# Performance work log

Measured on AMD Instinct MI355X. Metric: run time of the kernel, lower is better.

The kernel has to match this reference:

```python
import jax, jax.numpy as jnp
import numpy as np

B, N, M = 16, 4096, 1024
INPUT_DIM, COND_DIM = 512, 512
HEADS, DIM_HEAD = 8, 64
HIDDEN = HEADS * DIM_HEAD


def setup_inputs() -> dict:
    key = jax.random.key(0)
    ks = jax.random.split(key, 6)
    x = jax.random.normal(ks[0], (B, INPUT_DIM, N), dtype=jnp.float32)
    c = jax.random.normal(ks[1], (B, COND_DIM, M), dtype=jnp.float32)
    # 1x1 conv weights as [out_ch, in_ch] matrices
    Wq = jax.random.normal(ks[2], (HIDDEN, INPUT_DIM), dtype=jnp.float32) * (INPUT_DIM ** -0.5)
    Wkv = jax.random.normal(ks[3], (2 * HIDDEN, COND_DIM), dtype=jnp.float32) * (COND_DIM ** -0.5)
    Wo = jax.random.normal(ks[4], (INPUT_DIM, HIDDEN), dtype=jnp.float32) * (HIDDEN ** -0.5)
    bo = jax.random.normal(ks[5], (INPUT_DIM,), dtype=jnp.float32) * 0.01
    return {"x": x, "c": c, "Wq": Wq, "Wkv": Wkv, "Wo": Wo, "bo": bo}


def reference(x, c, Wq, Wkv, Wo, bo):
    scale = DIM_HEAD ** -0.5
    # 1x1 convs == channel-mixing matmuls
    q = jnp.einsum('bcn,oc->bon', x, Wq)            # [B, HIDDEN, N]
    kv = jnp.einsum('bcm,oc->bom', c, Wkv)          # [B, 2*HIDDEN, M]
    k, v = jnp.split(kv, 2, axis=1)                 # each [B, HIDDEN, M]
    # split heads: b (h d) n -> b h d n
    q = q.reshape(B, HEADS, DIM_HEAD, N) * scale
    k = k.reshape(B, HEADS, DIM_HEAD, M)
    v = v.reshape(B, HEADS, DIM_HEAD, M)
    # softmax over conditioning sequence dim
    k = jax.nn.softmax(k, axis=-1)
    # context: [B, H, d, e] (dim_head x dim_head)
    context = jnp.einsum('bhdm,bhem->bhde', k, v)
    # out: [B, H, e, N]
    out = jnp.einsum('bhde,bhdn->bhen', context, q)
    out = out.reshape(B, HIDDEN, N)
    return jnp.einsum('bcn,oc->bon', out, Wo) + bo[None, :, None]
```

## Files before the change

### kernel.cpp

```cpp
#include <hip/hip_runtime.h>

#define KDIM 512

typedef __attribute__((ext_vector_type(8))) short bf16x8;
typedef __attribute__((ext_vector_type(4))) float f32x4;
typedef unsigned short u16;
typedef unsigned int u32;

static __device__ __forceinline__ u16 f2bf(float f) {
  u32 u = __builtin_bit_cast(u32, f);
  u32 r = u + 0x7fffu + ((u >> 16) & 1u);
  return (u16)(r >> 16);
}
static __device__ __forceinline__ bf16x8 ld_frag(const u16* p) {
  uint2 lo = *(const uint2*)p;
  uint2 hi = *(const uint2*)(p + 4);
  uint4 u = make_uint4(lo.x, lo.y, hi.x, hi.y);
  return __builtin_bit_cast(bf16x8, u);
}

__global__ __launch_bounds__(256) void cvt_f32_bf16(
    const float* __restrict__ src, u16* __restrict__ dst, int n8)
{
  int i = blockIdx.x * 256 + threadIdx.x;
  if (i >= n8) return;
  float4 a = *(const float4*)(src + (long)i * 8);
  float4 b = *(const float4*)(src + (long)i * 8 + 4);
  u32 w0 = (u32)f2bf(a.x) | ((u32)f2bf(a.y) << 16);
  u32 w1 = (u32)f2bf(a.z) | ((u32)f2bf(a.w) << 16);
  u32 w2 = (u32)f2bf(b.x) | ((u32)f2bf(b.y) << 16);
  u32 w3 = (u32)f2bf(b.z) | ((u32)f2bf(b.w) << 16);
  *(uint4*)(dst + (long)i * 8) = make_uint4(w0, w1, w2, w3);
}

template<bool OUT_BF16, bool BIAS, bool CLUST>
__global__ __launch_bounds__(512, 2) void gemm_bm512(
    const u16* __restrict__ Ap, long a_bstride,
    const float* __restrict__ Bp, long b_bstride,
    void* __restrict__ Op, long o_bstride,
    const float* __restrict__ bias, int ldn)
{
  constexpr int LDT = 68;
  __shared__ u16 Ash[512 * LDT];
  __shared__ u16 Bsh[128 * LDT];

  int mt, nt, b;
  if constexpr (CLUST) {
    const int bx = blockIdx.x;
    const int xcd = bx & 7, idx = bx >> 3;
    b = xcd + 8 * (idx >> 5);
    nt = idx & 31;
    mt = 0;
  } else {
    mt = blockIdx.x; nt = blockIdx.y; b = blockIdx.z;
  }
  const long mtile = (long)mt * 512;
  const long ntile = (long)nt * 128;
  const u16* Ab = Ap + (long)b * a_bstride + mtile * KDIM;
  const float* Bb = Bp + (long)b * b_bstride + ntile;

  const int t = threadIdx.x;
  const int lane = t & 63, wv = t >> 6;
  const int wm = wv >> 1, wn = wv & 1;
  const int lrow = lane & 15, lkh = lane >> 4;

  const int arow = t >> 3, akc = t & 7;
  const int nq = t & 31;
  const int kq = ((t >> 5) ^ ((t >> 2) & 7)) & 15;

  f32x4 acc[8][4] = {};
  uint4 pa[8];
  float4 pb[4];

  #pragma unroll
  for (int i = 0; i < 8; ++i)
    pa[i] = *(const uint4*)(Ab + (long)(arow + i * 64) * KDIM + akc * 8);
  #pragma unroll
  for (int kk = 0; kk < 4; ++kk)
    pb[kk] = *(const float4*)(Bb + (long)(kq * 4 + kk) * ldn + nq * 4);

  #pragma unroll
  for (int i = 0; i < 8; ++i) {
    u16* dst = &Ash[(arow + i * 64) * LDT + akc * 8];
    *(uint2*)dst       = make_uint2(pa[i].x, pa[i].y);
    *(uint2*)(dst + 4) = make_uint2(pa[i].z, pa[i].w);
  }
  {
    float r0[4] = {pb[0].x, pb[0].y, pb[0].z, pb[0].w};
    float r1[4] = {pb[1].x, pb[1].y, pb[1].z, pb[1].w};
    float r2[4] = {pb[2].x, pb[2].y, pb[2].z, pb[2].w};
    float r3[4] = {pb[3].x, pb[3].y, pb[3].z, pb[3].w};
    #pragma unroll
    for (int jj = 0; jj < 4; ++jj) {
      u32 w0 = (u32)f2bf(r0[jj]) | ((u32)f2bf(r1[jj]) << 16);
      u32 w1 = (u32)f2bf(r2[jj]) | ((u32)f2bf(r3[jj]) << 16);
      *(uint2*)&Bsh[(nq * 4 + jj) * LDT + kq * 4] = make_uint2(w0, w1);
    }
  }
  __syncthreads();

  for (int kt8 = 0; kt8 < 8; ++kt8) {
    const bool more = kt8 < 7;
    if (more) {
      const int kt = (kt8 + 1) * 64;
      #pragma unroll
      for (int i = 0; i < 8; ++i)
        pa[i] = *(const uint4*)(Ab + (long)(arow + i * 64) * KDIM + kt + akc * 8);
      #pragma unroll
      for (int kk = 0; kk < 4; ++kk)
        pb[kk] = *(const float4*)(Bb + (long)(kt + kq * 4 + kk) * ldn + nq * 4);
    }
    #pragma unroll
    for (int kk = 0; kk < 2; ++kk) {
      bf16x8 bfr[4];
      #pragma unroll
      for (int ni = 0; ni < 4; ++ni)
        bfr[ni] = ld_frag(&Bsh[(wn * 64 + ni * 16 + lrow) * LDT + kk * 32 + lkh * 8]);
      #pragma unroll
      for (int mi = 0; mi < 8; ++mi) {
        bf16x8 af = ld_frag(&Ash[(wm * 128 + mi * 16 + lrow) * LDT + kk * 32 + lkh * 8]);
        #pragma unroll
        for (int ni = 0; ni < 4; ++ni)
          acc[mi][ni] = __builtin_amdgcn_mfma_f32_16x16x32_bf16(af, bfr[ni], acc[mi][ni], 0, 0, 0);
      }
    }
    __syncthreads();
    if (more) {
      #pragma unroll
      for (int i = 0; i < 8; ++i) {
        u16* dst = &Ash[(arow + i * 64) * LDT + akc * 8];
        *(uint2*)dst       = make_uint2(pa[i].x, pa[i].y);
        *(uint2*)(dst + 4) = make_uint2(pa[i].z, pa[i].w);
      }
      float r0[4] = {pb[0].x, pb[0].y, pb[0].z, pb[0].w};
      float r1[4] = {pb[1].x, pb[1].y, pb[1].z, pb[1].w};
      float r2[4] = {pb[2].x, pb[2].y, pb[2].z, pb[2].w};
      float r3[4] = {pb[3].x, pb[3].y, pb[3].z, pb[3].w};
      #pragma unroll
      for (int jj = 0; jj < 4; ++jj) {
        u32 w0 = (u32)f2bf(r0[jj]) | ((u32)f2bf(r1[jj]) << 16);
        u32 w1 = (u32)f2bf(r2[jj]) | ((u32)f2bf(r3[jj]) << 16);
        *(uint2*)&Bsh[(nq * 4 + jj) * LDT + kq * 4] = make_uint2(w0, w1);
      }
      __syncthreads();
    }
  }

  #pragma unroll
  for (int mi = 0; mi < 8; ++mi) {
    #pragma unroll
    for (int r = 0; r < 4; ++r) {
      long gr = mtile + wm * 128 + mi * 16 + lkh * 4 + r;
      float bv = 0.0f;
      if constexpr (BIAS) bv = bias[gr];
      #pragma unroll
      for (int ni = 0; ni < 4; ++ni) {
        long gc = ntile + wn * 64 + ni * 16 + lrow;
        float v = acc[mi][ni][r] + bv;
        if constexpr (OUT_BF16)
          ((u16*)Op)[(long)b * o_bstride + gr * ldn + gc] = f2bf(v);
        else
          ((float*)Op)[(long)b * o_bstride + gr * ldn + gc] = v;
      }
    }
  }
}

__global__ __launch_bounds__(256, 2) void softmax_context(
    const u16* __restrict__ kv, float* __restrict__ ctx)
{
  constexpr int LDE = 132;
  __shared__ float rowmax[64], rowinv[64];
  __shared__ u16 Ke[64 * LDE];
  __shared__ u16 Vs[64 * LDE];
  __shared__ float pr[64 * 68];

  const int bh = blockIdx.x;
  const u16* Kr = kv + (long)(bh >> 3) * (1024 * 1024) + (long)(bh & 7) * (64 * 1024);
  const u16* Vr = Kr + 512 * 1024;

  const int t = threadIdx.x;
  const int lane = t & 63, wv = t >> 6;
  const int lrow = lane & 15, lkh = lane >> 4;
  const int d4 = t >> 2, q4 = t & 3;

  {
    const u16* row = Kr + d4 * 1024 + q4 * 256;
    float mx = -3e38f;
    for (int i = 0; i < 256; i += 8) {
      uint4 v = *(const uint4*)(row + i);
      u32 ws[4] = {v.x, v.y, v.z, v.w};
      #pragma unroll
      for (int j = 0; j < 4; ++j) {
        mx = fmaxf(mx, __builtin_bit_cast(float, ws[j] << 16));
        mx = fmaxf(mx, __builtin_bit_cast(float, ws[j] & 0xffff0000u));
      }
    }
    mx = fmaxf(mx, __shfl_xor(mx, 1));
    mx = fmaxf(mx, __shfl_xor(mx, 2));
    float s = 0.f;
    for (int i = 0; i < 256; i += 8) {
      uint4 v = *(const uint4*)(row + i);
      u32 ws[4] = {v.x, v.y, v.z, v.w};
      #pragma unroll
      for (int j = 0; j < 4; ++j) {
        s += __expf(__builtin_bit_cast(float, ws[j] << 16) - mx);
        s += __expf(__builtin_bit_cast(float, ws[j] & 0xffff0000u) - mx);
      }
    }
    s += __shfl_xor(s, 1);
    s += __shfl_xor(s, 2);
    if (q4 == 0) { rowmax[d4] = mx; rowinv[d4] = 1.f / s; }
  }
  __syncthreads();

  f32x4 cacc[4][4] = {};

  for (int mc = 0; mc < 8; ++mc) {
    {
      int dd = t >> 2, j = t & 3;
      int m0 = mc * 128 + j * 32;
      float mx = rowmax[dd], inv = rowinv[dd];
      const u16* src = Kr + dd * 1024 + m0;
      u16* dst = &Ke[dd * LDE + j * 32];
      #pragma unroll
      for (int cq = 0; cq < 4; ++cq) {
        uint4 v = *(const uint4*)(src + cq * 8);
        u32 in[4] = {v.x, v.y, v.z, v.w};
        u32 out[4];
        #pragma unroll
        for (int j2 = 0; j2 < 4; ++j2) {
          float lo = __builtin_bit_cast(float, in[j2] << 16);
          float hi = __builtin_bit_cast(float, in[j2] & 0xffff0000u);
          out[j2] = (u32)f2bf(__expf(lo - mx) * inv) |
                    ((u32)f2bf(__expf(hi - mx) * inv) << 16);
        }
        *(uint2*)(dst + cq * 8)     = make_uint2(out[0], out[1]);
        *(uint2*)(dst + cq * 8 + 4) = make_uint2(out[2], out[3]);
      }
      const u16* vsrc = Vr + dd * 1024 + m0;
      u16* vdst = &Vs[dd * LDE + j * 32];
      #pragma unroll
      for (int cq = 0; cq < 4; ++cq) {
        uint4 v = *(const uint4*)(vsrc + cq * 8);
        *(uint2*)(vdst + cq * 8)     = make_uint2(v.x, v.y);
        *(uint2*)(vdst + cq * 8 + 4) = make_uint2(v.z, v.w);
      }
    }
    __syncthreads();
    bf16x8 ka[4], vb[4];
    #pragma unroll
    for (int mi = 0; mi < 4; ++mi)
      ka[mi] = ld_frag(&Ke[(mi * 16 + lrow) * LDE + wv * 32 + lkh * 8]);
    #pragma unroll
    for (int ni = 0; ni < 4; ++ni)
      vb[ni] = ld_frag(&Vs[(ni * 16 + lrow) * LDE + wv * 32 + lkh * 8]);
    #pragma unroll
    for (int mi = 0; mi < 4; ++mi)
      #pragma unroll
      for (int ni = 0; ni < 4; ++ni)
        cacc[mi][ni] = __builtin_amdgcn_mfma_f32_16x16x32_bf16(ka[mi], vb[ni], cacc[mi][ni], 0, 0, 0);
    __syncthreads();
  }

  for (int w = 0; w < 4; ++w) {
    if (wv == w) {
      #pragma unroll
      for (int mi = 0; mi < 4; ++mi)
        #pragma unroll
        for (int ni = 0; ni < 4; ++ni)
          #pragma unroll
          for (int r = 0; r < 4; ++r) {
            float* p = &pr[(mi * 16 + lkh * 4 + r) * 68 + (ni * 16 + lrow)];
            float v = cacc[mi][ni][r];
            if (w == 0) *p = v; else *p += v;
          }
    }
    __syncthreads();
  }
  float* cg = ctx + (long)bh * 4096;
  for (int i = 0; i < 16; ++i) {
    int o = t + i * 256;
    cg[o] = 0.125f * pr[(o >> 6) * 68 + (o & 63)];
  }
}

__global__ __launch_bounds__(256) void compose_u(
    const float* __restrict__ ctx, const float* __restrict__ Wo, u16* __restrict__ U)
{
  __shared__ float cs[16 * 64];
  const int bh = blockIdx.x, dq = blockIdx.y;
  const int b = bh >> 3, h = bh & 7;
  const int t = threadIdx.x;
  const float* cgrp = ctx + (long)bh * 4096 + dq * 16 * 64;
  for (int i = t; i < 1024; i += 256) cs[i] = cgrp[i];
  __syncthreads();
  #pragma unroll
  for (int rep = 0; rep < 2; ++rep) {
    int o = rep * 256 + t;
    const float* wrow = Wo + (long)o * 512 + h * 64;
    float acc[16] = {};
    for (int e = 0; e < 64; ++e) {
      float w = wrow[e];
      #pragma unroll
      for (int dd = 0; dd < 16; ++dd) acc[dd] += w * cs[dd * 64 + e];
    }
    u16* urow = U + (long)b * (512 * 512) + (long)o * 512 + h * 64 + dq * 16;
    #pragma unroll
    for (int dd = 0; dd < 16; ++dd) urow[dd] = f2bf(acc[dd]);
  }
}

extern "C" void kernel_launch(void* const* d_in, const int* in_sizes, int n_in,
                              void* d_out, int out_size, void* d_ws, size_t ws_size,
                              hipStream_t stream)
{
  const float* x   = (const float*)d_in[0];
  const float* c   = (const float*)d_in[1];
  const float* Wq  = (const float*)d_in[2];
  const float* Wkv = (const float*)d_in[3];
  const float* Wo  = (const float*)d_in[4];
  const float* bo  = (const float*)d_in[5];

  char* ws = (char*)d_ws;
  u16*   kv   = (u16*)ws;
  float* ctx  = (float*)(ws + 33554432);
  u16*   U    = (u16*)(ws + 35651584);
  u16*   Weff = (u16*)(ws + 44040192);
  u16*   Wkvb = (u16*)(ws + 44040192);

  cvt_f32_bf16<<<dim3(256), 256, 0, stream>>>(Wkv, Wkvb, 65536);
  gemm_bm512<true, false, false><<<dim3(2, 8, 16), 512, 0, stream>>>(
      Wkvb, 0, c, 512L * 1024, kv, 1024L * 1024, nullptr, 1024);
  softmax_context<<<dim3(128), 256, 0, stream>>>(kv, ctx);
  compose_u<<<dim3(128, 4), 256, 0, stream>>>(ctx, Wo, U);
  gemm_bm512<true, false, false><<<dim3(1, 4, 16), 512, 0, stream>>>(
      U, 512L * 512, Wq, 0, Weff, 512L * 512, nullptr, 512);
  gemm_bm512<false, true, true><<<dim3(512), 512, 0, stream>>>(
      Weff, 512L * 512, x, 512L * 4096, d_out, 512L * 4096, bo, 4096);
}
```

Before: 189.2 us.

## Rewrite GEMM with double-buffered swizzled LDS, wave priority, and staged epilogue

Replaces the single-buffer padded LDS GEMM with a 32-wide-K double-buffered pipeline. Tiles are stored with an XOR swizzle so fragments load as single 128-bit LDS reads. MFMA blocks are wrapped in s_setprio. The epilogue now stages accumulators through LDS so global stores are row-contiguous and vectorized, which targets the scattered scalar output writes. In exchange it uses more LDS (80KB) and adds extra barriers in the epilogue.

```diff
diff --git a/kernel.cpp b/kernel.cpp
--- a/kernel.cpp
+++ b/kernel.cpp
@@ -11,12 +11,6 @@
   u32 u = __builtin_bit_cast(u32, f);
   u32 r = u + 0x7fffu + ((u >> 16) & 1u);
   return (u16)(r >> 16);
-}
-static __device__ __forceinline__ bf16x8 ld_frag(const u16* p) {
-  uint2 lo = *(const uint2*)p;
-  uint2 hi = *(const uint2*)(p + 4);
-  uint4 u = make_uint4(lo.x, lo.y, hi.x, hi.y);
-  return __builtin_bit_cast(bf16x8, u);
 }
 
 __global__ __launch_bounds__(256) void cvt_f32_bf16(
@@ -33,27 +27,60 @@
   *(uint4*)(dst + (long)i * 8) = make_uint4(w0, w1, w2, w3);
 }
 
+#define AOFF(row, c16) ((((row) * 32) + (c16)) ^ (((row) & 7) << 3))
+
+#define LOADA(dst, kt) { _Pragma("unroll") \
+  for (int i_ = 0; i_ < 4; ++i_) \
+    dst[i_] = *(const uint4*)(Ab + (long)(ar + i_ * 128) * KDIM + (kt) + ac * 8); }
+
+#define LOADB(d0, d1, kt) { \
+  d0 = *(const float4*)(Bb + (long)((kt) + kq2)     * ldn + nq * 4); \
+  d1 = *(const float4*)(Bb + (long)((kt) + kq2 + 1) * ldn + nq * 4); }
+
+#define STAGEA(src, base) { _Pragma("unroll") \
+  for (int i_ = 0; i_ < 4; ++i_) \
+    *(uint4*)&lds[(base) + AOFF(ar + i_ * 128, ac * 8)] = src[i_]; }
+
+#define STAGEB(s0, s1, base) { \
+  float q0_[4] = {s0.x, s0.y, s0.z, s0.w}; \
+  float q1_[4] = {s1.x, s1.y, s1.z, s1.w}; \
+  _Pragma("unroll") for (int j_ = 0; j_ < 4; ++j_) { \
+    int n_ = nq * 4 + j_; \
+    u32 w_ = (u32)f2bf(q0_[j_]) | ((u32)f2bf(q1_[j_]) << 16); \
+    *(u32*)&lds[(base) + AOFF(n_, kq2)] = w_; } }
+
+#define MFMA_STEP(abase, bbase) { \
+  bf16x8 bfr_[4]; \
+  _Pragma("unroll") for (int ni_ = 0; ni_ < 4; ++ni_) { \
+    int n_ = wn * 64 + ni_ * 16 + lrow; \
+    bfr_[ni_] = *(const bf16x8*)&lds[(bbase) + AOFF(n_, lkh * 8)]; } \
+  __builtin_amdgcn_s_setprio(1); \
+  _Pragma("unroll") for (int mi_ = 0; mi_ < 8; ++mi_) { \
+    int rr_ = wm * 128 + mi_ * 16 + lrow; \
+    bf16x8 af_ = *(const bf16x8*)&lds[(abase) + AOFF(rr_, lkh * 8)]; \
+    _Pragma("unroll") for (int ni_ = 0; ni_ < 4; ++ni_) \
+      acc[mi_][ni_] = __builtin_amdgcn_mfma_f32_16x16x32_bf16(af_, bfr_[ni_], acc[mi_][ni_], 0, 0, 0); } \
+  __builtin_amdgcn_s_setprio(0); }
+
 template<bool OUT_BF16, bool BIAS, bool CLUST>
-__global__ __launch_bounds__(512, 2) void gemm_bm512(
+__global__ __launch_bounds__(512, 2) void gemm_v2(
     const u16* __restrict__ Ap, long a_bstride,
     const float* __restrict__ Bp, long b_bstride,
     void* __restrict__ Op, long o_bstride,
     const float* __restrict__ bias, int ldn)
 {
-  constexpr int LDT = 68;
-  __shared__ u16 Ash[512 * LDT];
-  __shared__ u16 Bsh[128 * LDT];
+  __shared__ char RAW[81920];
+  u16* lds = (u16*)RAW;
 
   int mt, nt, b;
   if constexpr (CLUST) {
     const int bx = blockIdx.x;
-    const int xcd = bx & 7, idx = bx >> 3;
-    b = xcd + 8 * (idx >> 5);
+    const int idx = bx >> 3;
+    b = (bx & 7) + 8 * (idx >> 5);
     nt = idx & 31;
     mt = 0;
-  } else {
-    mt = blockIdx.x; nt = blockIdx.y; b = blockIdx.z;
-  }
+  } else { mt = blockIdx.x; nt = blockIdx.y; b = blockIdx.z; }
+
   const long mtile = (long)mt * 512;
   const long ntile = (long)nt * 128;
   const u16* Ab = Ap + (long)b * a_bstride + mtile * KDIM;
@@ -64,106 +91,77 @@
   const int wm = wv >> 1, wn = wv & 1;
   const int lrow = lane & 15, lkh = lane >> 4;
 
-  const int arow = t >> 3, akc = t & 7;
+  const int ar = t >> 2, ac = t & 3;
   const int nq = t & 31;
-  const int kq = ((t >> 5) ^ ((t >> 2) & 7)) & 15;
+  const int kq2 = (t >> 5) * 2;
 
   f32x4 acc[8][4] = {};
-  uint4 pa[8];
-  float4 pb[4];
-
-  #pragma unroll
-  for (int i = 0; i < 8; ++i)
-    pa[i] = *(const uint4*)(Ab + (long)(arow + i * 64) * KDIM + akc * 8);
-  #pragma unroll
-  for (int kk = 0; kk < 4; ++kk)
-    pb[kk] = *(const float4*)(Bb + (long)(kq * 4 + kk) * ldn + nq * 4);
-
-  #pragma unroll
-  for (int i = 0; i < 8; ++i) {
-    u16* dst = &Ash[(arow + i * 64) * LDT + akc * 8];
-    *(uint2*)dst       = make_uint2(pa[i].x, pa[i].y);
-    *(uint2*)(dst + 4) = make_uint2(pa[i].z, pa[i].w);
-  }
-  {
-    float r0[4] = {pb[0].x, pb[0].y, pb[0].z, pb[0].w};
-    float r1[4] = {pb[1].x, pb[1].y, pb[1].z, pb[1].w};
-    float r2[4] = {pb[2].x, pb[2].y, pb[2].z, pb[2].w};
-    float r3[4] = {pb[3].x, pb[3].y, pb[3].z, pb[3].w};
-    #pragma unroll
-    for (int jj = 0; jj < 4; ++jj) {
-      u32 w0 = (u32)f2bf(r0[jj]) | ((u32)f2bf(r1[jj]) << 16);
-      u32 w1 = (u32)f2bf(r2[jj]) | ((u32)f2bf(r3[jj]) << 16);
-      *(uint2*)&Bsh[(nq * 4 + jj) * LDT + kq * 4] = make_uint2(w0, w1);
-    }
-  }
+  uint4 a0[4], a1[4];
+  float4 b0a, b0b, b1a, b1b;
+
+  LOADA(a0, 0)  LOADB(b0a, b0b, 0)
+  LOADA(a1, 32) LOADB(b1a, b1b, 32)
+  STAGEA(a0, 0) STAGEB(b0a, b0b, 32768)
   __syncthreads();
 
-  for (int kt8 = 0; kt8 < 8; ++kt8) {
-    const bool more = kt8 < 7;
+  for (int s2 = 0; s2 < 8; ++s2) {
+    const int kt = s2 * 64;
+    const bool more = s2 < 7;
+    if (more) { LOADA(a0, kt + 64) LOADB(b0a, b0b, kt + 64) }
+    MFMA_STEP(0, 32768)
+    STAGEA(a1, 16384) STAGEB(b1a, b1b, 36864)
+    __syncthreads();
+    if (more) { LOADA(a1, kt + 96) LOADB(b1a, b1b, kt + 96) }
+    MFMA_STEP(16384, 36864)
     if (more) {
-      const int kt = (kt8 + 1) * 64;
-      #pragma unroll
-      for (int i = 0; i < 8; ++i)
-        pa[i] = *(const uint4*)(Ab + (long)(arow + i * 64) * KDIM + kt + akc * 8);
-      #pragma unroll
-      for (int kk = 0; kk < 4; ++kk)
-        pb[kk] = *(const float4*)(Bb + (long)(kt + kq * 4 + kk) * ldn + nq * 4);
-    }
-    #pragma unroll
-    for (int kk = 0; kk < 2; ++kk) {
-      bf16x8 bfr[4];
-      #pragma unroll
-      for (int ni = 0; ni < 4; ++ni)
-        bfr[ni] = ld_frag(&Bsh[(wn * 64 + ni * 16 + lrow) * LDT + kk * 32 + lkh * 8]);
-      #pragma unroll
-      for (int mi = 0; mi < 8; ++mi) {
-        bf16x8 af = ld_frag(&Ash[(wm * 128 + mi * 16 + lrow) * LDT + kk * 32 + lkh * 8]);
-        #pragma unroll
-        for (int ni = 0; ni < 4; ++ni)
-          acc[mi][ni] = __builtin_amdgcn_mfma_f32_16x16x32_bf16(af, bfr[ni], acc[mi][ni], 0, 0, 0);
-      }
-    }
-    __syncthreads();
-    if (more) {
-      #pragma unroll
-      for (int i = 0; i < 8; ++i) {
-        u16* dst = &Ash[(arow + i * 64) * LDT + akc * 8];
-        *(uint2*)dst       = make_uint2(pa[i].x, pa[i].y);
-        *(uint2*)(dst + 4) = make_uint2(pa[i].z, pa[i].w);
-      }
-      float r0[4] = {pb[0].x, pb[0].y, pb[0].z, pb[0].w};
-      float r1[4] = {pb[1].x, pb[1].y, pb[1].z, pb[1].w};
-      float r2[4] = {pb[2].x, pb[2].y, pb[2].z, pb[2].w};
-      float r3[4] = {pb[3].x, pb[3].y, pb[3].z, pb[3].w};
-      #pragma unroll
-      for (int jj = 0; jj < 4; ++jj) {
-        u32 w0 = (u32)f2bf(r0[jj]) | ((u32)f2bf(r1[jj]) << 16);
-        u32 w1 = (u32)f2bf(r2[jj]) | ((u32)f2bf(r3[jj]) << 16);
-        *(uint2*)&Bsh[(nq * 4 + jj) * LDT + kq * 4] = make_uint2(w0, w1);
-      }
+      STAGEA(a0, 0) STAGEB(b0a, b0b, 32768)
       __syncthreads();
     }
   }
 
+  float* ldsF = (float*)RAW;
+  const int L = t >> 3, seg = (t & 7) * 16;
+  const int erow = wm * 16 + lkh * 4;
+  const int ecol = wn * 64 + lrow;
   #pragma unroll
   for (int mi = 0; mi < 8; ++mi) {
-    #pragma unroll
-    for (int r = 0; r < 4; ++r) {
-      long gr = mtile + wm * 128 + mi * 16 + lkh * 4 + r;
-      float bv = 0.0f;
-      if constexpr (BIAS) bv = bias[gr];
-      #pragma unroll
-      for (int ni = 0; ni < 4; ++ni) {
-        long gc = ntile + wn * 64 + ni * 16 + lrow;
-        float v = acc[mi][ni][r] + bv;
-        if constexpr (OUT_BF16)
-          ((u16*)Op)[(long)b * o_bstride + gr * ldn + gc] = f2bf(v);
-        else
-          ((float*)Op)[(long)b * o_bstride + gr * ldn + gc] = v;
-      }
-    }
-  }
+    __syncthreads();
+    #pragma unroll
+    for (int ni = 0; ni < 4; ++ni)
+      #pragma unroll
+      for (int r = 0; r < 4; ++r)
+        ldsF[(erow + r) * 132 + ecol + ni * 16] = acc[mi][ni][r];
+    __syncthreads();
+    const long gr = mtile + (L >> 4) * 128 + mi * 16 + (L & 15);
+    float bv = 0.f;
+    if constexpr (BIAS) bv = bias[gr];
+    float v[16];
+    #pragma unroll
+    for (int j = 0; j < 16; ++j) v[j] = ldsF[L * 132 + seg + j] + bv;
+    if constexpr (OUT_BF16) {
+      u32 w[8];
+      #pragma unroll
+      for (int j = 0; j < 8; ++j)
+        w[j] = (u32)f2bf(v[2 * j]) | ((u32)f2bf(v[2 * j + 1]) << 16);
+      u16* dst = (u16*)Op + (long)b * o_bstride + gr * ldn + ntile + seg;
+      *(uint4*)dst       = make_uint4(w[0], w[1], w[2], w[3]);
+      *(uint4*)(dst + 8) = make_uint4(w[4], w[5], w[6], w[7]);
+    } else {
+      float* dst = (float*)Op + (long)b * o_bstride + gr * ldn + ntile + seg;
+      *(float4*)dst        = make_float4(v[0],  v[1],  v[2],  v[3]);
+      *(float4*)(dst + 4)  = make_float4(v[4],  v[5],  v[6],  v[7]);
+      *(float4*)(dst + 8)  = make_float4(v[8],  v[9],  v[10], v[11]);
+      *(float4*)(dst + 12) = make_float4(v[12], v[13], v[14], v[15]);
+    }
+  }
+}
+
+typedef __attribute__((ext_vector_type(8))) short bf16x8_t;
+static __device__ __forceinline__ bf16x8 ld_frag2(const u16* p) {
+  uint2 lo = *(const uint2*)p;
+  uint2 hi = *(const uint2*)(p + 4);
+  uint4 u = make_uint4(lo.x, lo.y, hi.x, hi.y);
+  return __builtin_bit_cast(bf16x8, u);
 }
 
 __global__ __launch_bounds__(256, 2) void softmax_context(
@@ -251,10 +249,10 @@
     bf16x8 ka[4], vb[4];
     #pragma unroll
     for (int mi = 0; mi < 4; ++mi)
-      ka[mi] = ld_frag(&Ke[(mi * 16 + lrow) * LDE + wv * 32 + lkh * 8]);
+      ka[mi] = ld_frag2(&Ke[(mi * 16 + lrow) * LDE + wv * 32 + lkh * 8]);
     #pragma unroll
     for (int ni = 0; ni < 4; ++ni)
-      vb[ni] = ld_frag(&Vs[(ni * 16 + lrow) * LDE + wv * 32 + lkh * 8]);
+      vb[ni] = ld_frag2(&Vs[(ni * 16 + lrow) * LDE + wv * 32 + lkh * 8]);
     #pragma unroll
     for (int mi = 0; mi < 4; ++mi)
       #pragma unroll
@@ -330,12 +328,12 @@
   u16*   Wkvb = (u16*)(ws + 44040192);
 
   cvt_f32_bf16<<<dim3(256), 256, 0, stream>>>(Wkv, Wkvb, 65536);
-  gemm_bm512<true, false, false><<<dim3(2, 8, 16), 512, 0, stream>>>(
+  gemm_v2<true, false, false><<<dim3(2, 8, 16), 512, 0, stream>>>(
       Wkvb, 0, c, 512L * 1024, kv, 1024L * 1024, nullptr, 1024);
   softmax_context<<<dim3(128), 256, 0, stream>>>(kv, ctx);
   compose_u<<<dim3(128, 4), 256, 0, stream>>>(ctx, Wo, U);
-  gemm_bm512<true, false, false><<<dim3(1, 4, 16), 512, 0, stream>>>(
+  gemm_v2<true, false, false><<<dim3(1, 4, 16), 512, 0, stream>>>(
       U, 512L * 512, Wq, 0, Weff, 512L * 512, nullptr, 512);
-  gemm_bm512<false, true, true><<<dim3(512), 512, 0, stream>>>(
+  gemm_v2<false, true, true><<<dim3(512), 512, 0, stream>>>(
       Weff, 512L * 512, x, 512L * 4096, d_out, 512L * 4096, bo, 4096);
 }
```

New measurement: 344.2 us. +82.0%, slower.

## Shrink GEMM M-tile to 256 rows and raise occupancy with flattened grid

Applied to the files above, without the earlier changes.

Replaces the 512-row GEMM tile with a 256-row tile, halving accumulators and A staging registers and LDS per block, and raises launch bounds to 4 blocks per CU. The grid is flattened to a 1D index ordered by M-tile, then N-tile, then batch, which drops the XCD-aware clustering used for the final GEMM. It also removes the XOR swizzle on the B staging index. The aim is more resident waves and more blocks per launch to hide memory latency, at the cost of reloading each B tile for twice as many M-tiles and possibly more LDS bank conflicts on B stores.

```diff
diff --git a/kernel.cpp b/kernel.cpp
--- a/kernel.cpp
+++ b/kernel.cpp
@@ -33,28 +33,22 @@
   *(uint4*)(dst + (long)i * 8) = make_uint4(w0, w1, w2, w3);
 }
 
-template<bool OUT_BF16, bool BIAS, bool CLUST>
-__global__ __launch_bounds__(512, 2) void gemm_bm512(
+template<bool OUT_BF16, bool BIAS, int MT, int NT>
+__global__ __launch_bounds__(512, 4) void gemm_v3(
     const u16* __restrict__ Ap, long a_bstride,
     const float* __restrict__ Bp, long b_bstride,
     void* __restrict__ Op, long o_bstride,
     const float* __restrict__ bias, int ldn)
 {
   constexpr int LDT = 68;
-  __shared__ u16 Ash[512 * LDT];
+  __shared__ u16 Ash[256 * LDT];
   __shared__ u16 Bsh[128 * LDT];
 
-  int mt, nt, b;
-  if constexpr (CLUST) {
-    const int bx = blockIdx.x;
-    const int xcd = bx & 7, idx = bx >> 3;
-    b = xcd + 8 * (idx >> 5);
-    nt = idx & 31;
-    mt = 0;
-  } else {
-    mt = blockIdx.x; nt = blockIdx.y; b = blockIdx.z;
-  }
-  const long mtile = (long)mt * 512;
+  const int d = blockIdx.x;
+  const int mt = d % MT;
+  const int nt = (d / MT) % NT;
+  const int b  = d / (MT * NT);
+  const long mtile = (long)mt * 256;
   const long ntile = (long)nt * 128;
   const u16* Ab = Ap + (long)b * a_bstride + mtile * KDIM;
   const float* Bb = Bp + (long)b * b_bstride + ntile;
@@ -64,52 +58,42 @@
   const int wm = wv >> 1, wn = wv & 1;
   const int lrow = lane & 15, lkh = lane >> 4;
 
-  const int arow = t >> 3, akc = t & 7;
+  const int ar = t >> 3, ac8 = t & 7;
   const int nq = t & 31;
-  const int kq = ((t >> 5) ^ ((t >> 2) & 7)) & 15;
-
-  f32x4 acc[8][4] = {};
-  uint4 pa[8];
+  const int kq = t >> 5;
+
+  f32x4 acc[4][4] = {};
+  uint4 pa[4];
   float4 pb[4];
 
-  #pragma unroll
-  for (int i = 0; i < 8; ++i)
-    pa[i] = *(const uint4*)(Ab + (long)(arow + i * 64) * KDIM + akc * 8);
-  #pragma unroll
-  for (int kk = 0; kk < 4; ++kk)
-    pb[kk] = *(const float4*)(Bb + (long)(kq * 4 + kk) * ldn + nq * 4);
-
-  #pragma unroll
-  for (int i = 0; i < 8; ++i) {
-    u16* dst = &Ash[(arow + i * 64) * LDT + akc * 8];
-    *(uint2*)dst       = make_uint2(pa[i].x, pa[i].y);
-    *(uint2*)(dst + 4) = make_uint2(pa[i].z, pa[i].w);
-  }
-  {
-    float r0[4] = {pb[0].x, pb[0].y, pb[0].z, pb[0].w};
-    float r1[4] = {pb[1].x, pb[1].y, pb[1].z, pb[1].w};
-    float r2[4] = {pb[2].x, pb[2].y, pb[2].z, pb[2].w};
-    float r3[4] = {pb[3].x, pb[3].y, pb[3].z, pb[3].w};
-    #pragma unroll
-    for (int jj = 0; jj < 4; ++jj) {
-      u32 w0 = (u32)f2bf(r0[jj]) | ((u32)f2bf(r1[jj]) << 16);
-      u32 w1 = (u32)f2bf(r2[jj]) | ((u32)f2bf(r3[jj]) << 16);
-      *(uint2*)&Bsh[(nq * 4 + jj) * LDT + kq * 4] = make_uint2(w0, w1);
-    }
-  }
+  #define LOADA_V3(kt) { _Pragma("unroll") \
+    for (int i_ = 0; i_ < 4; ++i_) \
+      pa[i_] = *(const uint4*)(Ab + (long)(ar + i_ * 64) * KDIM + (kt) + ac8 * 8); }
+
+  #define LOADB_V3(kt) { _Pragma("unroll") \
+    for (int k_ = 0; k_ < 4; ++k_) \
+      pb[k_] = *(const float4*)(Bb + (long)((kt) + kq * 4 + k_) * ldn + nq * 4); }
+
+  #define STAGE_V3() { \
+    _Pragma("unroll") for (int i_ = 0; i_ < 4; ++i_) { \
+      u16* dst_ = &Ash[(ar + i_ * 64) * LDT + ac8 * 8]; \
+      *(uint2*)dst_       = make_uint2(pa[i_].x, pa[i_].y); \
+      *(uint2*)(dst_ + 4) = make_uint2(pa[i_].z, pa[i_].w); } \
+    float q0_[4] = {pb[0].x, pb[0].y, pb[0].z, pb[0].w}; \
+    float q1_[4] = {pb[1].x, pb[1].y, pb[1].z, pb[1].w}; \
+    float q2_[4] = {pb[2].x, pb[2].y, pb[2].z, pb[2].w}; \
+    float q3_[4] = {pb[3].x, pb[3].y, pb[3].z, pb[3].w}; \
+    _Pragma("unroll") for (int j_ = 0; j_ < 4; ++j_) { \
+      u32 w0_ = (u32)f2bf(q0_[j_]) | ((u32)f2bf(q1_[j_]) << 16); \
+      u32 w1_ = (u32)f2bf(q2_[j_]) | ((u32)f2bf(q3_[j_]) << 16); \
+      *(uint2*)&Bsh[(nq * 4 + j_) * LDT + kq * 4] = make_uint2(w0_, w1_); } }
+
+  LOADA_V3(0) LOADB_V3(0)
+  STAGE_V3()
   __syncthreads();
 
-  for (int kt8 = 0; kt8 < 8; ++kt8) {
-    const bool more = kt8 < 7;
-    if (more) {
-      const int kt = (kt8 + 1) * 64;
-      #pragma unroll
-      for (int i = 0; i < 8; ++i)
-        pa[i] = *(const uint4*)(Ab + (long)(arow + i * 64) * KDIM + kt + akc * 8);
-      #pragma unroll
-      for (int kk = 0; kk < 4; ++kk)
-        pb[kk] = *(const float4*)(Bb + (long)(kt + kq * 4 + kk) * ldn + nq * 4);
-    }
+  for (int s = 0; s < 8; ++s) {
+    if (s < 7) { LOADA_V3((s + 1) * 64) LOADB_V3((s + 1) * 64) }
     #pragma unroll
     for (int kk = 0; kk < 2; ++kk) {
       bf16x8 bfr[4];
@@ -117,40 +101,25 @@
       for (int ni = 0; ni < 4; ++ni)
         bfr[ni] = ld_frag(&Bsh[(wn * 64 + ni * 16 + lrow) * LDT + kk * 32 + lkh * 8]);
       #pragma unroll
-      for (int mi = 0; mi < 8; ++mi) {
-        bf16x8 af = ld_frag(&Ash[(wm * 128 + mi * 16 + lrow) * LDT + kk * 32 + lkh * 8]);
+      for (int mi = 0; mi < 4; ++mi) {
+        bf16x8 af = ld_frag(&Ash[(wm * 64 + mi * 16 + lrow) * LDT + kk * 32 + lkh * 8]);
         #pragma unroll
         for (int ni = 0; ni < 4; ++ni)
           acc[mi][ni] = __builtin_amdgcn_mfma_f32_16x16x32_bf16(af, bfr[ni], acc[mi][ni], 0, 0, 0);
       }
     }
     __syncthreads();
-    if (more) {
-      #pragma unroll
-      for (int i = 0; i < 8; ++i) {
-        u16* dst = &Ash[(arow + i * 64) * LDT + akc * 8];
-        *(uint2*)dst       = make_uint2(pa[i].x, pa[i].y);
-        *(uint2*)(dst + 4) = make_uint2(pa[i].z, pa[i].w);
-      }
-      float r0[4] = {pb[0].x, pb[0].y, pb[0].z, pb[0].w};
-      float r1[4] = {pb[1].x, pb[1].y, pb[1].z, pb[1].w};
-      float r2[4] = {pb[2].x, pb[2].y, pb[2].z, pb[2].w};
-      float r3[4] = {pb[3].x, pb[3].y, pb[3].z, pb[3].w};
-      #pragma unroll
-      for (int jj = 0; jj < 4; ++jj) {
-        u32 w0 = (u32)f2bf(r0[jj]) | ((u32)f2bf(r1[jj]) << 16);
-        u32 w1 = (u32)f2bf(r2[jj]) | ((u32)f2bf(r3[jj]) << 16);
-        *(uint2*)&Bsh[(nq * 4 + jj) * LDT + kq * 4] = make_uint2(w0, w1);
-      }
+    if (s < 7) {
+      STAGE_V3()
       __syncthreads();
     }
   }
 
   #pragma unroll
-  for (int mi = 0; mi < 8; ++mi) {
+  for (int mi = 0; mi < 4; ++mi) {
     #pragma unroll
     for (int r = 0; r < 4; ++r) {
-      long gr = mtile + wm * 128 + mi * 16 + lkh * 4 + r;
+      long gr = mtile + wm * 64 + mi * 16 + lkh * 4 + r;
       float bv = 0.0f;
       if constexpr (BIAS) bv = bias[gr];
       #pragma unroll
@@ -164,6 +133,9 @@
       }
     }
   }
+  #undef LOADA_V3
+  #undef LOADB_V3
+  #undef STAGE_V3
 }
 
 __global__ __launch_bounds__(256, 2) void softmax_context(
@@ -330,12 +302,12 @@
   u16*   Wkvb = (u16*)(ws + 44040192);
 
   cvt_f32_bf16<<<dim3(256), 256, 0, stream>>>(Wkv, Wkvb, 65536);
-  gemm_bm512<true, false, false><<<dim3(2, 8, 16), 512, 0, stream>>>(
+  gemm_v3<true, false, 4, 8><<<dim3(4 * 8 * 16), 512, 0, stream>>>(
       Wkvb, 0, c, 512L * 1024, kv, 1024L * 1024, nullptr, 1024);
   softmax_context<<<dim3(128), 256, 0, stream>>>(kv, ctx);
   compose_u<<<dim3(128, 4), 256, 0, stream>>>(ctx, Wo, U);
-  gemm_bm512<true, false, false><<<dim3(1, 4, 16), 512, 0, stream>>>(
+  gemm_v3<true, false, 2, 4><<<dim3(2 * 4 * 16), 512, 0, stream>>>(
       U, 512L * 512, Wq, 0, Weff, 512L * 512, nullptr, 512);
-  gemm_bm512<false, true, true><<<dim3(512), 512, 0, stream>>>(
+  gemm_v3<false, true, 2, 32><<<dim3(2 * 32 * 16), 512, 0, stream>>>(
       Weff, 512L * 512, x, 512L * 4096, d_out, 512L * 4096, bo, 4096);
 }
```

New measurement: 195.4 us. +3.3%, slower.
